# Kernel tuning notes

Hardware: AMD Instinct MI355X
Metric: run time of the kernel (lower is better)

## Reference

```python
import jax, jax.numpy as jnp
import numpy as np

N_NODES = 100000
N_EDGES = 1600000
IN_C = 128
HID = 128
N_TRUCKS = 32


def _graph_conv(x, src, dst, W_rel, b_rel, W_root):
    # PyG GraphConv: out_i = lin_rel(sum_{j in N(i)} x_j) + lin_root(x_i)
    agg = jax.ops.segment_sum(x[src], dst, num_segments=N_NODES)  # [N, C_in]
    return agg @ W_rel + b_rel + x @ W_root


def setup_inputs() -> dict:
    key = jax.random.key(0)
    ks = jax.random.split(key, 12)
    s_in = 1.0 / np.sqrt(IN_C)
    s_h = 1.0 / np.sqrt(HID)
    x = jax.random.normal(ks[0], (N_NODES, IN_C), dtype=jnp.float32)
    edge_index = jax.random.randint(ks[1], (2, N_EDGES), 0, N_NODES, dtype=jnp.int32)
    inp = {"x": x, "edge_index": edge_index}
    # conv layer 0: in -> hid
    inp["W_rel0"] = jax.random.normal(ks[2], (IN_C, HID), jnp.float32) * s_in
    inp["b_rel0"] = jnp.zeros((HID,), jnp.float32)
    inp["W_root0"] = jax.random.normal(ks[3], (IN_C, HID), jnp.float32) * s_in
    # conv layers 1, 2: hid -> hid
    inp["W_rel1"] = jax.random.normal(ks[4], (HID, HID), jnp.float32) * s_h
    inp["b_rel1"] = jnp.zeros((HID,), jnp.float32)
    inp["W_root1"] = jax.random.normal(ks[5], (HID, HID), jnp.float32) * s_h
    inp["W_rel2"] = jax.random.normal(ks[6], (HID, HID), jnp.float32) * s_h
    inp["b_rel2"] = jnp.zeros((HID,), jnp.float32)
    inp["W_root2"] = jax.random.normal(ks[7], (HID, HID), jnp.float32) * s_h
    # edge classifier: Linear(hid,hid) -> ReLU -> Linear(hid,n_trucks)
    inp["Wc0"] = jax.random.normal(ks[8], (HID, HID), jnp.float32) * s_h
    inp["bc0"] = jnp.zeros((HID,), jnp.float32)
    inp["Wc1"] = jax.random.normal(ks[9], (HID, N_TRUCKS), jnp.float32) * s_h
    inp["bc1"] = jnp.zeros((N_TRUCKS,), jnp.float32)
    return inp


def reference(x, edge_index, W_rel0, b_rel0, W_root0, W_rel1, b_rel1, W_root1,
              W_rel2, b_rel2, W_root2, Wc0, bc0, Wc1, bc1):
    src, dst = edge_index[0], edge_index[1]
    h = jax.nn.relu(_graph_conv(x, src, dst, W_rel0, b_rel0, W_root0))
    h = jax.nn.relu(_graph_conv(h, src, dst, W_rel1, b_rel1, W_root1))
    h = jax.nn.relu(_graph_conv(h, src, dst, W_rel2, b_rel2, W_root2))
    # dropout = identity in eval mode
    h = jax.nn.relu(h @ Wc0 + bc0)
    logits = h @ Wc1 + bc1  # [N, num_trucks]
    return logits
```

## Files before the change

kernel.cpp:

```cpp
#include <hip/hip_runtime.h>
#include <cstdint>

#define N_NODES 100000
#define N_EDGES 1600000
#define HID 128
#define NT 32

#define BSHIFT 7
#define NB 782
#define NBLK_B 512
#define EPB 3328
#define ITER_B 13
#define CAP 2560

typedef __attribute__((ext_vector_type(8))) short short8v;
typedef __attribute__((ext_vector_type(4))) float f32x4;
typedef __attribute__((ext_vector_type(4))) unsigned uint4v;

__device__ inline unsigned short f2bf(float f) {
    union { float f; unsigned u; } v; v.f = f;
    unsigned r = v.u + 0x7FFF + ((v.u >> 16) & 1);
    return (unsigned short)(r >> 16);
}
__device__ inline float bf2f(unsigned short u) {
    union { unsigned u; float f; } v; v.u = ((unsigned)u) << 16; return v.f;
}
__device__ inline float bflo(unsigned v) { return bf2f((unsigned short)(v & 0xFFFF)); }
__device__ inline float bfhi(unsigned v) { return bf2f((unsigned short)(v >> 16)); }

__global__ __launch_bounds__(256) void k_bscatter2(const int* __restrict__ src,
                                                   const int* __restrict__ dst,
                                                   int* __restrict__ gcur,
                                                   unsigned* __restrict__ staged, int n) {
    __shared__ int lh[NB];
    __shared__ int lbase[NB];
    const int t = threadIdx.x;
    for (int i = t; i < NB; i += 256) lh[i] = 0;
    __syncthreads();
    const int base = blockIdx.x * EPB;
    #pragma unroll 1
    for (int i = 0; i < ITER_B; ++i) {
        int e = base + i * 256 + t;
        if (e < n) atomicAdd(&lh[dst[e] >> BSHIFT], 1);
    }
    __syncthreads();
    for (int i = t; i < NB; i += 256) {
        int c = lh[i];
        lbase[i] = c ? atomicAdd(&gcur[i], c) : 0;
        lh[i] = 0;
    }
    __syncthreads();
    #pragma unroll 1
    for (int i = 0; i < ITER_B; ++i) {
        int e = base + i * 256 + t;
        if (e < n) {
            int d = dst[e];
            int b = d >> BSHIFT;
            int pos = lbase[b] + atomicAdd(&lh[b], 1);
            if (pos < CAP)
                staged[(size_t)b * CAP + pos] = (unsigned)src[e] | ((unsigned)(d & 127) << 17);
        }
    }
}

__global__ __launch_bounds__(256) void k_bgroup2(const unsigned* __restrict__ staged,
                                                 const int* __restrict__ gcur,
                                                 int* __restrict__ offsets,
                                                 int* __restrict__ deg,
                                                 int* __restrict__ csr) {
    __shared__ int lh[128];
    __shared__ int lex[128];
    const int t = threadIdx.x;
    const int b = blockIdx.x;
    const int s0 = b * CAP;
    int cnt = gcur[b];
    if (cnt > CAP) cnt = CAP;
    if (t < 128) lh[t] = 0;
    __syncthreads();
    for (int i = t; i < cnt; i += 256)
        atomicAdd(&lh[staged[(size_t)s0 + i] >> 17], 1);
    __syncthreads();
    int myc = (t < 128) ? lh[t] : 0;
    if (t < 128) lex[t] = myc;
    __syncthreads();
    #pragma unroll 1
    for (int d = 1; d < 128; d <<= 1) {
        int add = 0;
        if (t < 128 && t >= d) add = lex[t - d];
        __syncthreads();
        if (t < 128) lex[t] += add;
        __syncthreads();
    }
    if (t < 128) {
        int excl = lex[t] - myc;
        lex[t] = excl;
        int node = (b << BSHIFT) + t;
        if (node < N_NODES) {
            offsets[node] = s0 + excl;
            deg[node] = myc;
        }
        lh[t] = 0;
    }
    __syncthreads();
    for (int i = t; i < cnt; i += 256) {
        unsigned v = staged[(size_t)s0 + i];
        int local = v >> 17;
        int p = s0 + lex[local] + atomicAdd(&lh[local], 1);
        csr[p] = (int)(v & 0x1FFFF);
    }
}

__global__ void k_cast(const float* __restrict__ in, unsigned short* __restrict__ out, int n8) {
    int i = blockIdx.x * 256 + threadIdx.x;
    if (i >= n8) return;
    const float4* p = reinterpret_cast<const float4*>(in + (size_t)i * 8);
    float4 a = p[0], b = p[1];
    union { unsigned short u[8]; uint4v v; } o;
    o.u[0] = f2bf(a.x); o.u[1] = f2bf(a.y); o.u[2] = f2bf(a.z); o.u[3] = f2bf(a.w);
    o.u[4] = f2bf(b.x); o.u[5] = f2bf(b.y); o.u[6] = f2bf(b.z); o.u[7] = f2bf(b.w);
    *reinterpret_cast<uint4v*>(out + (size_t)i * 8) = o.v;
}

struct WPrepArgs {
    const float* src[7];
    unsigned short* dst[7];
    int Ndim[7];
};

__global__ void k_prep_w(WPrepArgs a) {
    int m = blockIdx.x;
    const float* s = a.src[m];
    unsigned short* d = a.dst[m];
    int N = a.Ndim[m];
    int total = 128 * N;
    for (int idx = threadIdx.x; idx < total; idx += 256) {
        int n = idx >> 7;
        int k = idx & 127;
        d[n * 128 + k] = f2bf(s[(size_t)k * N + n]);
    }
}

__global__ __launch_bounds__(256) void k_agg_w(const unsigned short* __restrict__ X,
                                               const int* __restrict__ offsets,
                                               const int* __restrict__ deg,
                                               const int* __restrict__ csr,
                                               unsigned short* __restrict__ agg, int n) {
    int node = blockIdx.x * 4 + (threadIdx.x >> 6);
    if (node >= n) return;
    const int lane = threadIdx.x & 63;
    const int q = lane >> 4;
    const int c = lane & 15;
    const int e0 = offsets[node];
    const int e1 = e0 + deg[node];

    float s[8];
    #pragma unroll
    for (int j = 0; j < 8; ++j) s[j] = 0.f;

    int e = e0 + q;
    for (; e + 12 < e1; e += 16) {
        int i0 = csr[e];
        int i1 = csr[e + 4];
        int i2 = csr[e + 8];
        int i3 = csr[e + 12];
        uint4v v0 = *reinterpret_cast<const uint4v*>(X + (size_t)i0 * 128 + c * 8);
        uint4v v1 = *reinterpret_cast<const uint4v*>(X + (size_t)i1 * 128 + c * 8);
        uint4v v2 = *reinterpret_cast<const uint4v*>(X + (size_t)i2 * 128 + c * 8);
        uint4v v3 = *reinterpret_cast<const uint4v*>(X + (size_t)i3 * 128 + c * 8);
        #pragma unroll
        for (int j = 0; j < 4; ++j) {
            s[2 * j]     += (bflo(v0[j]) + bflo(v1[j])) + (bflo(v2[j]) + bflo(v3[j]));
            s[2 * j + 1] += (bfhi(v0[j]) + bfhi(v1[j])) + (bfhi(v2[j]) + bfhi(v3[j]));
        }
    }
    for (; e < e1; e += 4) {
        int i0 = csr[e];
        uint4v v0 = *reinterpret_cast<const uint4v*>(X + (size_t)i0 * 128 + c * 8);
        #pragma unroll
        for (int j = 0; j < 4; ++j) {
            s[2 * j]     += bflo(v0[j]);
            s[2 * j + 1] += bfhi(v0[j]);
        }
    }
    #pragma unroll
    for (int m = 16; m < 64; m <<= 1) {
        #pragma unroll
        for (int j = 0; j < 8; ++j) s[j] += __shfl_xor(s[j], m, 64);
    }
    if (q == 0) {
        union { unsigned short u[8]; uint4v v; } o;
        #pragma unroll
        for (int j = 0; j < 8; ++j) o.u[j] = f2bf(s[j]);
        *reinterpret_cast<uint4v*>(agg + (size_t)node * 128 + c * 8) = o.v;
    }
}

__global__ __launch_bounds__(256) void k_mfma128(
    const unsigned short* __restrict__ Xa, const unsigned short* __restrict__ WtA,
    const unsigned short* __restrict__ Xb, const unsigned short* __restrict__ WtB,
    const float* __restrict__ bias, unsigned short* __restrict__ Out,
    int M, int doRelu)
{
    __shared__ unsigned short wlds[128 * 136];

    const int t = threadIdx.x;
    const int lane = t & 63;
    const int w = t >> 6;
    const int r0 = blockIdx.x * 128;
    const int lrow = lane & 15;
    const int kg = lane >> 4;

    f32x4 acc[2][8];
    #pragma unroll
    for (int i = 0; i < 2; ++i)
        #pragma unroll
        for (int f = 0; f < 8; ++f) acc[i][f] = (f32x4){0.f, 0.f, 0.f, 0.f};

    #pragma unroll 1
    for (int sidx = 0; sidx < 2; ++sidx) {
        const unsigned short* X  = sidx ? Xb : Xa;
        const unsigned short* Wt = sidx ? WtB : WtA;
        if (!X) break;
        __syncthreads();
        {
            int n = t >> 1;
            int half = (t & 1) * 64;
            const unsigned short* srcp = Wt + (size_t)n * 128 + half;
            unsigned short* dstp = &wlds[n * 136 + half];
            #pragma unroll
            for (int j = 0; j < 8; ++j)
                *reinterpret_cast<uint4v*>(dstp + j * 8) =
                    *reinterpret_cast<const uint4v*>(srcp + j * 8);
        }
        __syncthreads();
        #pragma unroll 1
        for (int kc = 0; kc < 4; ++kc) {
            const int kb = kc * 32 + kg * 8;
            short8v a0 = {0,0,0,0,0,0,0,0}, a1 = {0,0,0,0,0,0,0,0};
            int row0 = r0 + w * 32 + lrow;
            int row1 = row0 + 16;
            if (row0 < M) a0 = *reinterpret_cast<const short8v*>(X + (size_t)row0 * 128 + kb);
            if (row1 < M) a1 = *reinterpret_cast<const short8v*>(X + (size_t)row1 * 128 + kb);
            #pragma unroll
            for (int f = 0; f < 8; ++f) {
                short8v b = *reinterpret_cast<const short8v*>(&wlds[(f * 16 + lrow) * 136 + kb]);
                acc[0][f] = __builtin_amdgcn_mfma_f32_16x16x32_bf16(a0, b, acc[0][f], 0, 0, 0);
                acc[1][f] = __builtin_amdgcn_mfma_f32_16x16x32_bf16(a1, b, acc[1][f], 0, 0, 0);
            }
        }
    }
    #pragma unroll
    for (int rr = 0; rr < 2; ++rr) {
        #pragma unroll
        for (int f = 0; f < 8; ++f) {
            int col = f * 16 + lrow;
            float bv = bias[col];
            #pragma unroll
            for (int reg = 0; reg < 4; ++reg) {
                int row = r0 + w * 32 + rr * 16 + kg * 4 + reg;
                if (row < M) {
                    float v = acc[rr][f][reg] + bv;
                    if (doRelu) v = fmaxf(v, 0.f);
                    Out[(size_t)row * 128 + col] = f2bf(v);
                }
            }
        }
    }
}

__global__ __launch_bounds__(256) void k_tail(
    const unsigned short* __restrict__ Xa, const unsigned short* __restrict__ WtA,
    const unsigned short* __restrict__ Xb, const unsigned short* __restrict__ WtB,
    const float* __restrict__ bias,
    const unsigned short* __restrict__ WtC0, const float* __restrict__ bc0,
    const unsigned short* __restrict__ WtC1, const float* __restrict__ bc1,
    float* __restrict__ Out, int M)
{
    __shared__ unsigned short alds[128 * 136];
    __shared__ unsigned short wlds[128 * 136];

    const int t = threadIdx.x;
    const int lane = t & 63;
    const int w = t >> 6;
    const int r0 = blockIdx.x * 128;
    const int lrow = lane & 15;
    const int kg = lane >> 4;

    f32x4 acc[2][8];
    #pragma unroll
    for (int i = 0; i < 2; ++i)
        #pragma unroll
        for (int f = 0; f < 8; ++f) acc[i][f] = (f32x4){0.f, 0.f, 0.f, 0.f};

    #pragma unroll 1
    for (int sidx = 0; sidx < 2; ++sidx) {
        const unsigned short* X  = sidx ? Xb : Xa;
        const unsigned short* Wt = sidx ? WtB : WtA;
        __syncthreads();
        {
            int n = t >> 1;
            int half = (t & 1) * 64;
            const unsigned short* srcp = Wt + (size_t)n * 128 + half;
            unsigned short* dstp = &wlds[n * 136 + half];
            #pragma unroll
            for (int j = 0; j < 8; ++j)
                *reinterpret_cast<uint4v*>(dstp + j * 8) =
                    *reinterpret_cast<const uint4v*>(srcp + j * 8);
        }
        __syncthreads();
        #pragma unroll 1
        for (int kc = 0; kc < 4; ++kc) {
            const int kb = kc * 32 + kg * 8;
            short8v a0 = {0,0,0,0,0,0,0,0}, a1 = {0,0,0,0,0,0,0,0};
            int row0 = r0 + w * 32 + lrow;
            int row1 = row0 + 16;
            if (row0 < M) a0 = *reinterpret_cast<const short8v*>(X + (size_t)row0 * 128 + kb);
            if (row1 < M) a1 = *reinterpret_cast<const short8v*>(X + (size_t)row1 * 128 + kb);
            #pragma unroll
            for (int f = 0; f < 8; ++f) {
                short8v b = *reinterpret_cast<const short8v*>(&wlds[(f * 16 + lrow) * 136 + kb]);
                acc[0][f] = __builtin_amdgcn_mfma_f32_16x16x32_bf16(a0, b, acc[0][f], 0, 0, 0);
                acc[1][f] = __builtin_amdgcn_mfma_f32_16x16x32_bf16(a1, b, acc[1][f], 0, 0, 0);
            }
        }
    }
    __syncthreads();
    #pragma unroll
    for (int rr = 0; rr < 2; ++rr) {
        #pragma unroll
        for (int f = 0; f < 8; ++f) {
            int col = f * 16 + lrow;
            float bv = bias[col];
            #pragma unroll
            for (int reg = 0; reg < 4; ++reg) {
                int row = w * 32 + rr * 16 + kg * 4 + reg;
                alds[row * 136 + col] = f2bf(fmaxf(acc[rr][f][reg] + bv, 0.f));
            }
        }
    }
    {
        int n = t >> 1;
        int half = (t & 1) * 64;
        const unsigned short* srcp = WtC0 + (size_t)n * 128 + half;
        unsigned short* dstp = &wlds[n * 136 + half];
        #pragma unroll
        for (int j = 0; j < 8; ++j)
            *reinterpret_cast<uint4v*>(dstp + j * 8) =
                *reinterpret_cast<const uint4v*>(srcp + j * 8);
    }
    __syncthreads();

    f32x4 acc2[2][8];
    #pragma unroll
    for (int i = 0; i < 2; ++i)
        #pragma unroll
        for (int f = 0; f < 8; ++f) acc2[i][f] = (f32x4){0.f, 0.f, 0.f, 0.f};
    #pragma unroll 1
    for (int kc = 0; kc < 4; ++kc) {
        const int kb = kc * 32 + kg * 8;
        short8v a0 = *reinterpret_cast<const short8v*>(&alds[(w * 32 + lrow) * 136 + kb]);
        short8v a1 = *reinterpret_cast<const short8v*>(&alds[(w * 32 + 16 + lrow) * 136 + kb]);
        #pragma unroll
        for (int f = 0; f < 8; ++f) {
            short8v b = *reinterpret_cast<const short8v*>(&wlds[(f * 16 + lrow) * 136 + kb]);
            acc2[0][f] = __builtin_amdgcn_mfma_f32_16x16x32_bf16(a0, b, acc2[0][f], 0, 0, 0);
            acc2[1][f] = __builtin_amdgcn_mfma_f32_16x16x32_bf16(a1, b, acc2[1][f], 0, 0, 0);
        }
    }
    __syncthreads();

    #pragma unroll
    for (int rr = 0; rr < 2; ++rr) {
        #pragma unroll
        for (int f = 0; f < 8; ++f) {
            int col = f * 16 + lrow;
            float bv = bc0[col];
            #pragma unroll
            for (int reg = 0; reg < 4; ++reg) {
                int row = w * 32 + rr * 16 + kg * 4 + reg;
                alds[row * 136 + col] = f2bf(fmaxf(acc2[rr][f][reg] + bv, 0.f));
            }
        }
    }
    {
        int n = t >> 3;
        int seg = (t & 7) * 16;
        *reinterpret_cast<uint4v*>(&wlds[n * 136 + seg]) =
            *reinterpret_cast<const uint4v*>(WtC1 + (size_t)n * 128 + seg);
        *reinterpret_cast<uint4v*>(&wlds[n * 136 + seg + 8]) =
            *reinterpret_cast<const uint4v*>(WtC1 + (size_t)n * 128 + seg + 8);
    }
    __syncthreads();

    f32x4 acc3[2][2];
    #pragma unroll
    for (int i = 0; i < 2; ++i)
        #pragma unroll
        for (int f = 0; f < 2; ++f) acc3[i][f] = (f32x4){0.f, 0.f, 0.f, 0.f};
    #pragma unroll 1
    for (int kc = 0; kc < 4; ++kc) {
        const int kb = kc * 32 + kg * 8;
        short8v a0 = *reinterpret_cast<const short8v*>(&alds[(w * 32 + lrow) * 136 + kb]);
        short8v a1 = *reinterpret_cast<const short8v*>(&alds[(w * 32 + 16 + lrow) * 136 + kb]);
        #pragma unroll
        for (int f = 0; f < 2; ++f) {
            short8v b = *reinterpret_cast<const short8v*>(&wlds[(f * 16 + lrow) * 136 + kb]);
            acc3[0][f] = __builtin_amdgcn_mfma_f32_16x16x32_bf16(a0, b, acc3[0][f], 0, 0, 0);
            acc3[1][f] = __builtin_amdgcn_mfma_f32_16x16x32_bf16(a1, b, acc3[1][f], 0, 0, 0);
        }
    }
    #pragma unroll
    for (int rr = 0; rr < 2; ++rr) {
        #pragma unroll
        for (int f = 0; f < 2; ++f) {
            int col = f * 16 + lrow;
            float bv = bc1[col];
            #pragma unroll
            for (int reg = 0; reg < 4; ++reg) {
                int row = r0 + w * 32 + rr * 16 + kg * 4 + reg;
                if (row < M) Out[(size_t)row * 32 + col] = acc3[rr][f][reg] + bv;
            }
        }
    }
}

extern "C" void kernel_launch(void* const* d_in, const int* in_sizes, int n_in,
                              void* d_out, int out_size, void* d_ws, size_t ws_size,
                              hipStream_t stream) {
    (void)in_sizes; (void)n_in; (void)out_size; (void)ws_size;

    const float* x      = (const float*)d_in[0];
    const int*   ei     = (const int*)d_in[1];
    const float* Wrel0  = (const float*)d_in[2];
    const float* brel0  = (const float*)d_in[3];
    const float* Wroot0 = (const float*)d_in[4];
    const float* Wrel1  = (const float*)d_in[5];
    const float* brel1  = (const float*)d_in[6];
    const float* Wroot1 = (const float*)d_in[7];
    const float* Wrel2  = (const float*)d_in[8];
    const float* brel2  = (const float*)d_in[9];
    const float* Wroot2 = (const float*)d_in[10];
    const float* Wc0    = (const float*)d_in[11];
    const float* bc0    = (const float*)d_in[12];
    const float* Wc1    = (const float*)d_in[13];
    const float* bc1    = (const float*)d_in[14];

    const int* src = ei;
    const int* dst = ei + N_EDGES;

    char* w = (char*)d_ws;
    auto alloc = [&](size_t bytes) {
        char* p = w;
        w += (bytes + 255) & ~(size_t)255;
        return (void*)p;
    };
    int* gcur    = (int*)alloc((size_t)NB * 4);
    int* offsets = (int*)alloc((size_t)N_NODES * 4);
    int* deg     = (int*)alloc((size_t)N_NODES * 4);
    unsigned* staged = (unsigned*)alloc((size_t)NB * CAP * 4);
    int* csr     = (int*)alloc((size_t)NB * CAP * 4);
    unsigned short* x_bf   = (unsigned short*)alloc((size_t)N_NODES * HID * 2);
    unsigned short* agg_bf = (unsigned short*)alloc((size_t)N_NODES * HID * 2);
    unsigned short* hA     = (unsigned short*)alloc((size_t)N_NODES * HID * 2);
    unsigned short* hB     = (unsigned short*)alloc((size_t)N_NODES * HID * 2);
    unsigned short* wtRel0  = (unsigned short*)alloc(128 * 128 * 2);
    unsigned short* wtRoot0 = (unsigned short*)alloc(128 * 128 * 2);
    unsigned short* wtRel1  = (unsigned short*)alloc(128 * 128 * 2);
    unsigned short* wtRoot1 = (unsigned short*)alloc(128 * 128 * 2);
    unsigned short* wtRel2  = (unsigned short*)alloc(128 * 128 * 2);
    unsigned short* wtRoot2 = (unsigned short*)alloc(128 * 128 * 2);
    unsigned short* wtC0    = (unsigned short*)alloc(128 * 128 * 2);
    unsigned short* wtC1    = (unsigned short*)alloc(32 * 128 * 2);

    (void)hipMemsetAsync(gcur, 0, (size_t)NB * 4, stream);
    k_bscatter2<<<NBLK_B, 256, 0, stream>>>(src, dst, gcur, staged, N_EDGES);
    k_bgroup2<<<NB, 256, 0, stream>>>(staged, gcur, offsets, deg, csr);

    k_cast<<<(N_NODES * HID / 8 + 255) / 256, 256, 0, stream>>>(x, x_bf, N_NODES * HID / 8);
    {
        WPrepArgs a;
        a.src[0] = Wrel0;  a.dst[0] = wtRel0;  a.Ndim[0] = 128;
        a.src[1] = Wroot0; a.dst[1] = wtRoot0; a.Ndim[1] = 128;
        a.src[2] = Wrel1;  a.dst[2] = wtRel1;  a.Ndim[2] = 128;
        a.src[3] = Wroot1; a.dst[3] = wtRoot1; a.Ndim[3] = 128;
        a.src[4] = Wrel2;  a.dst[4] = wtRel2;  a.Ndim[4] = 128;
        a.src[5] = Wroot2; a.dst[5] = wtRoot2; a.Ndim[5] = 128;
        a.src[6] = Wc0;    a.dst[6] = wtC0;    a.Ndim[6] = 128;
        k_prep_w<<<7, 256, 0, stream>>>(a);
        WPrepArgs b;
        b.src[0] = Wc1; b.dst[0] = wtC1; b.Ndim[0] = 32;
        for (int i = 1; i < 7; ++i) { b.src[i] = Wc1; b.dst[i] = wtC1; b.Ndim[i] = 32; }
        k_prep_w<<<1, 256, 0, stream>>>(b);
    }

    const int ab = (N_NODES + 3) / 4;
    const int gb = (N_NODES + 127) / 128;

    k_agg_w<<<ab, 256, 0, stream>>>(x_bf, offsets, deg, csr, agg_bf, N_NODES);
    k_mfma128<<<gb, 256, 0, stream>>>(agg_bf, wtRel0, x_bf, wtRoot0, brel0, hA, N_NODES, 1);
    k_agg_w<<<ab, 256, 0, stream>>>(hA, offsets, deg, csr, agg_bf, N_NODES);
    k_mfma128<<<gb, 256, 0, stream>>>(agg_bf, wtRel1, hA, wtRoot1, brel1, hB, N_NODES, 1);
    k_agg_w<<<ab, 256, 0, stream>>>(hB, offsets, deg, csr, agg_bf, N_NODES);
    k_tail<<<gb, 256, 0, stream>>>(agg_bf, wtRel2, hB, wtRoot2, brel2,
                                   wtC0, bc0, wtC1, bc1, (float*)d_out, N_NODES);
}
```

Measured before the change: 356.4 us.

## Store node features in column-slab layout and aggregate one slab per block

Node feature matrices are stored as 8 slabs of 16 bf16 columns (32 bytes per node per slab) instead of row-major 128 columns. The aggregation kernel assigns each block to one slab, so every gather touches a 3.2 MB slab that can stay resident in cache instead of the full 25.6 MB feature matrix. CSR entries are pre-scaled to byte offsets, and nontemporal loads and stores are added. The GEMM kernels read and write the new layout. In exchange each edge is now read eight times and each gather fetches only 32 bytes, and the GEMM output stores become narrower scattered writes.

```diff
diff --git a/kernel.cpp b/kernel.cpp
--- a/kernel.cpp
+++ b/kernel.cpp
@@ -15,6 +15,7 @@
 
 typedef __attribute__((ext_vector_type(8))) short short8v;
 typedef __attribute__((ext_vector_type(4))) float f32x4;
+typedef __attribute__((ext_vector_type(2))) float f32x2;
 typedef __attribute__((ext_vector_type(4))) unsigned uint4v;
 
 __device__ inline unsigned short f2bf(float f) {
@@ -25,8 +26,9 @@
 __device__ inline float bf2f(unsigned short u) {
     union { unsigned u; float f; } v; v.u = ((unsigned)u) << 16; return v.f;
 }
-__device__ inline float bflo(unsigned v) { return bf2f((unsigned short)(v & 0xFFFF)); }
-__device__ inline float bfhi(unsigned v) { return bf2f((unsigned short)(v >> 16)); }
+__device__ inline float u2f(unsigned u) {
+    union { unsigned u; float f; } v; v.u = u; return v.f;
+}
 
 __global__ __launch_bounds__(256) void k_bscatter2(const int* __restrict__ src,
                                                    const int* __restrict__ dst,
@@ -106,19 +108,26 @@
         unsigned v = staged[(size_t)s0 + i];
         int local = v >> 17;
         int p = s0 + lex[local] + atomicAdd(&lh[local], 1);
-        csr[p] = (int)(v & 0x1FFFF);
-    }
-}
-
-__global__ void k_cast(const float* __restrict__ in, unsigned short* __restrict__ out, int n8) {
-    int i = blockIdx.x * 256 + threadIdx.x;
-    if (i >= n8) return;
-    const float4* p = reinterpret_cast<const float4*>(in + (size_t)i * 8);
-    float4 a = p[0], b = p[1];
-    union { unsigned short u[8]; uint4v v; } o;
-    o.u[0] = f2bf(a.x); o.u[1] = f2bf(a.y); o.u[2] = f2bf(a.z); o.u[3] = f2bf(a.w);
-    o.u[4] = f2bf(b.x); o.u[5] = f2bf(b.y); o.u[6] = f2bf(b.z); o.u[7] = f2bf(b.w);
-    *reinterpret_cast<uint4v*>(out + (size_t)i * 8) = o.v;
+        csr[p] = (int)((v & 0x1FFFF) << 5);
+    }
+}
+
+__global__ void k_cast_blk(const float* __restrict__ in, unsigned short* __restrict__ out, int n) {
+    int node = blockIdx.x * 256 + threadIdx.x;
+    if (node >= n) return;
+    const float4* p = reinterpret_cast<const float4*>(in + (size_t)node * 128);
+    #pragma unroll
+    for (int g = 0; g < 8; ++g) {
+        float4 a = p[g * 4 + 0], b = p[g * 4 + 1], c = p[g * 4 + 2], d = p[g * 4 + 3];
+        union { unsigned short u[16]; uint4v v[2]; } o;
+        o.u[0] = f2bf(a.x);  o.u[1] = f2bf(a.y);  o.u[2] = f2bf(a.z);  o.u[3] = f2bf(a.w);
+        o.u[4] = f2bf(b.x);  o.u[5] = f2bf(b.y);  o.u[6] = f2bf(b.z);  o.u[7] = f2bf(b.w);
+        o.u[8] = f2bf(c.x);  o.u[9] = f2bf(c.y);  o.u[10] = f2bf(c.z); o.u[11] = f2bf(c.w);
+        o.u[12] = f2bf(d.x); o.u[13] = f2bf(d.y); o.u[14] = f2bf(d.z); o.u[15] = f2bf(d.w);
+        uint4v* dp = reinterpret_cast<uint4v*>(out + ((size_t)g * n + node) * 16);
+        __builtin_nontemporal_store(o.v[0], dp);
+        __builtin_nontemporal_store(o.v[1], dp + 1);
+    }
 }
 
 struct WPrepArgs {
@@ -140,64 +149,53 @@
     }
 }
 
-__global__ __launch_bounds__(256) void k_agg_w(const unsigned short* __restrict__ X,
-                                               const int* __restrict__ offsets,
-                                               const int* __restrict__ deg,
-                                               const int* __restrict__ csr,
-                                               unsigned short* __restrict__ agg, int n) {
-    int node = blockIdx.x * 4 + (threadIdx.x >> 6);
+__global__ __launch_bounds__(256) void k_agg_cs(const unsigned short* __restrict__ Xp,
+                                                const int* __restrict__ offsets,
+                                                const int* __restrict__ deg,
+                                                const int* __restrict__ csr,
+                                                unsigned short* __restrict__ aggp, int n) {
+    const int g  = blockIdx.x & 7;
+    const int nb = blockIdx.x >> 3;
+    const int t  = threadIdx.x;
+    const int w  = t >> 6;
+    const int lane = t & 63;
+    const int nl = lane >> 5;
+    const int q  = (lane >> 3) & 3;
+    const int c  = lane & 7;
+    const int node = nb * 8 + w * 2 + nl;
     if (node >= n) return;
-    const int lane = threadIdx.x & 63;
-    const int q = lane >> 4;
-    const int c = lane & 15;
+
+    const char* Xg = reinterpret_cast<const char*>(Xp) + (size_t)g * n * 32 + c * 4;
     const int e0 = offsets[node];
     const int e1 = e0 + deg[node];
 
-    float s[8];
-    #pragma unroll
-    for (int j = 0; j < 8; ++j) s[j] = 0.f;
-
+    f32x2 a = (f32x2){0.f, 0.f};
     int e = e0 + q;
-    for (; e + 12 < e1; e += 16) {
-        int i0 = csr[e];
-        int i1 = csr[e + 4];
-        int i2 = csr[e + 8];
-        int i3 = csr[e + 12];
-        uint4v v0 = *reinterpret_cast<const uint4v*>(X + (size_t)i0 * 128 + c * 8);
-        uint4v v1 = *reinterpret_cast<const uint4v*>(X + (size_t)i1 * 128 + c * 8);
-        uint4v v2 = *reinterpret_cast<const uint4v*>(X + (size_t)i2 * 128 + c * 8);
-        uint4v v3 = *reinterpret_cast<const uint4v*>(X + (size_t)i3 * 128 + c * 8);
-        #pragma unroll
-        for (int j = 0; j < 4; ++j) {
-            s[2 * j]     += (bflo(v0[j]) + bflo(v1[j])) + (bflo(v2[j]) + bflo(v3[j]));
-            s[2 * j + 1] += (bfhi(v0[j]) + bfhi(v1[j])) + (bfhi(v2[j]) + bfhi(v3[j]));
-        }
-    }
-    for (; e < e1; e += 4) {
-        int i0 = csr[e];
-        uint4v v0 = *reinterpret_cast<const uint4v*>(X + (size_t)i0 * 128 + c * 8);
-        #pragma unroll
-        for (int j = 0; j < 4; ++j) {
-            s[2 * j]     += bflo(v0[j]);
-            s[2 * j + 1] += bfhi(v0[j]);
-        }
-    }
-    #pragma unroll
-    for (int m = 16; m < 64; m <<= 1) {
-        #pragma unroll
-        for (int j = 0; j < 8; ++j) s[j] += __shfl_xor(s[j], m, 64);
-    }
+    for (; e + 4 < e1; e += 8) {
+        int b0 = __builtin_nontemporal_load(csr + e);
+        int b1 = __builtin_nontemporal_load(csr + e + 4);
+        unsigned v0 = *reinterpret_cast<const unsigned*>(Xg + b0);
+        unsigned v1 = *reinterpret_cast<const unsigned*>(Xg + b1);
+        a += (f32x2){u2f(v0 << 16), u2f(v0 & 0xFFFF0000u)};
+        a += (f32x2){u2f(v1 << 16), u2f(v1 & 0xFFFF0000u)};
+    }
+    if (e < e1) {
+        int b0 = __builtin_nontemporal_load(csr + e);
+        unsigned v0 = *reinterpret_cast<const unsigned*>(Xg + b0);
+        a += (f32x2){u2f(v0 << 16), u2f(v0 & 0xFFFF0000u)};
+    }
+    a.x += __shfl_xor(a.x, 8, 64);  a.y += __shfl_xor(a.y, 8, 64);
+    a.x += __shfl_xor(a.x, 16, 64); a.y += __shfl_xor(a.y, 16, 64);
     if (q == 0) {
-        union { unsigned short u[8]; uint4v v; } o;
-        #pragma unroll
-        for (int j = 0; j < 8; ++j) o.u[j] = f2bf(s[j]);
-        *reinterpret_cast<uint4v*>(agg + (size_t)node * 128 + c * 8) = o.v;
+        unsigned pack = ((unsigned)f2bf(a.y) << 16) | (unsigned)f2bf(a.x);
+        unsigned* op = reinterpret_cast<unsigned*>(aggp) + ((size_t)g * n + node) * 8 + c;
+        __builtin_nontemporal_store(pack, op);
     }
 }
 
 __global__ __launch_bounds__(256) void k_mfma128(
-    const unsigned short* __restrict__ Xa, const unsigned short* __restrict__ WtA,
-    const unsigned short* __restrict__ Xb, const unsigned short* __restrict__ WtB,
+    const unsigned short* __restrict__ XaP, const unsigned short* __restrict__ WtA,
+    const unsigned short* __restrict__ XbP, const unsigned short* __restrict__ WtB,
     const float* __restrict__ bias, unsigned short* __restrict__ Out,
     int M, int doRelu)
 {
@@ -216,9 +214,13 @@
         #pragma unroll
         for (int f = 0; f < 8; ++f) acc[i][f] = (f32x4){0.f, 0.f, 0.f, 0.f};
 
+    const int row0 = r0 + w * 32 + lrow;
+    const int row1 = row0 + 16;
+    const int co = (kg & 1) * 8;
+
     #pragma unroll 1
     for (int sidx = 0; sidx < 2; ++sidx) {
-        const unsigned short* X  = sidx ? Xb : Xa;
+        const unsigned short* X  = sidx ? XbP : XaP;
         const unsigned short* Wt = sidx ? WtB : WtA;
         if (!X) break;
         __syncthreads();
@@ -236,11 +238,10 @@
         #pragma unroll 1
         for (int kc = 0; kc < 4; ++kc) {
             const int kb = kc * 32 + kg * 8;
+            const int g = kc * 2 + (kg >> 1);
             short8v a0 = {0,0,0,0,0,0,0,0}, a1 = {0,0,0,0,0,0,0,0};
-            int row0 = r0 + w * 32 + lrow;
-            int row1 = row0 + 16;
-            if (row0 < M) a0 = *reinterpret_cast<const short8v*>(X + (size_t)row0 * 128 + kb);
-            if (row1 < M) a1 = *reinterpret_cast<const short8v*>(X + (size_t)row1 * 128 + kb);
+            if (row0 < M) a0 = *reinterpret_cast<const short8v*>(X + ((size_t)g * M + row0) * 16 + co);
+            if (row1 < M) a1 = *reinterpret_cast<const short8v*>(X + ((size_t)g * M + row1) * 16 + co);
             #pragma unroll
             for (int f = 0; f < 8; ++f) {
                 short8v b = *reinterpret_cast<const short8v*>(&wlds[(f * 16 + lrow) * 136 + kb]);
@@ -261,7 +262,7 @@
                 if (row < M) {
                     float v = acc[rr][f][reg] + bv;
                     if (doRelu) v = fmaxf(v, 0.f);
-                    Out[(size_t)row * 128 + col] = f2bf(v);
+                    Out[((size_t)f * M + row) * 16 + lrow] = f2bf(v);
                 }
             }
         }
@@ -269,8 +270,8 @@
 }
 
 __global__ __launch_bounds__(256) void k_tail(
-    const unsigned short* __restrict__ Xa, const unsigned short* __restrict__ WtA,
-    const unsigned short* __restrict__ Xb, const unsigned short* __restrict__ WtB,
+    const unsigned short* __restrict__ XaP, const unsigned short* __restrict__ WtA,
+    const unsigned short* __restrict__ XbP, const unsigned short* __restrict__ WtB,
     const float* __restrict__ bias,
     const unsigned short* __restrict__ WtC0, const float* __restrict__ bc0,
     const unsigned short* __restrict__ WtC1, const float* __restrict__ bc1,
@@ -292,9 +293,13 @@
         #pragma unroll
         for (int f = 0; f < 8; ++f) acc[i][f] = (f32x4){0.f, 0.f, 0.f, 0.f};
 
+    const int row0g = r0 + w * 32 + lrow;
+    const int row1g = row0g + 16;
+    const int co = (kg & 1) * 8;
+
     #pragma unroll 1
     for (int sidx = 0; sidx < 2; ++sidx) {
-        const unsigned short* X  = sidx ? Xb : Xa;
+        const unsigned short* X  = sidx ? XbP : XaP;
         const unsigned short* Wt = sidx ? WtB : WtA;
         __syncthreads();
         {
@@ -311,11 +316,10 @@
         #pragma unroll 1
         for (int kc = 0; kc < 4; ++kc) {
             const int kb = kc * 32 + kg * 8;
+            const int g = kc * 2 + (kg >> 1);
             short8v a0 = {0,0,0,0,0,0,0,0}, a1 = {0,0,0,0,0,0,0,0};
-            int row0 = r0 + w * 32 + lrow;
-            int row1 = row0 + 16;
-            if (row0 < M) a0 = *reinterpret_cast<const short8v*>(X + (size_t)row0 * 128 + kb);
-            if (row1 < M) a1 = *reinterpret_cast<const short8v*>(X + (size_t)row1 * 128 + kb);
+            if (row0g < M) a0 = *reinterpret_cast<const short8v*>(X + ((size_t)g * M + row0g) * 16 + co);
+            if (row1g < M) a1 = *reinterpret_cast<const short8v*>(X + ((size_t)g * M + row1g) * 16 + co);
             #pragma unroll
             for (int f = 0; f < 8; ++f) {
                 short8v b = *reinterpret_cast<const short8v*>(&wlds[(f * 16 + lrow) * 136 + kb]);
@@ -476,7 +480,7 @@
     k_bscatter2<<<NBLK_B, 256, 0, stream>>>(src, dst, gcur, staged, N_EDGES);
     k_bgroup2<<<NB, 256, 0, stream>>>(staged, gcur, offsets, deg, csr);
 
-    k_cast<<<(N_NODES * HID / 8 + 255) / 256, 256, 0, stream>>>(x, x_bf, N_NODES * HID / 8);
+    k_cast_blk<<<(N_NODES + 255) / 256, 256, 0, stream>>>(x, x_bf, N_NODES);
     {
         WPrepArgs a;
         a.src[0] = Wrel0;  a.dst[0] = wtRel0;  a.Ndim[0] = 128;
@@ -493,14 +497,14 @@
         k_prep_w<<<1, 256, 0, stream>>>(b);
     }
 
-    const int ab = (N_NODES + 3) / 4;
+    const int ab = ((N_NODES + 7) / 8) * 8;
     const int gb = (N_NODES + 127) / 128;
 
-    k_agg_w<<<ab, 256, 0, stream>>>(x_bf, offsets, deg, csr, agg_bf, N_NODES);
+    k_agg_cs<<<ab, 256, 0, stream>>>(x_bf, offsets, deg, csr, agg_bf, N_NODES);
     k_mfma128<<<gb, 256, 0, stream>>>(agg_bf, wtRel0, x_bf, wtRoot0, brel0, hA, N_NODES, 1);
-    k_agg_w<<<ab, 256, 0, stream>>>(hA, offsets, deg, csr, agg_bf, N_NODES);
+    k_agg_cs<<<ab, 256, 0, stream>>>(hA, offsets, deg, csr, agg_bf, N_NODES);
     k_mfma128<<<gb, 256, 0, stream>>>(agg_bf, wtRel1, hA, wtRoot1, brel1, hB, N_NODES, 1);
-    k_agg_w<<<ab, 256, 0, stream>>>(hB, offsets, deg, csr, agg_bf, N_NODES);
+    k_agg_cs<<<ab, 256, 0, stream>>>(hB, offsets, deg, csr, agg_bf, N_NODES);
     k_tail<<<gb, 256, 0, stream>>>(agg_bf, wtRel2, hB, wtRoot2, brel2,
                                    wtC0, bc0, wtC1, bc1, (float*)d_out, N_NODES);
 }
```

Result: slower. 678.2 us (+90.3%).
